# Kernel optimization log

Hardware: AMD Instinct MI355X
Metric: run time of the kernel (lower is better)

## Reference

```python
import jax, jax.numpy as jnp
import numpy as np

N = 100000
E = 3200000
NFEAT = 256
NHID = 128
NCLASS = 16
TEXT_CNT = 50000


def setup_inputs() -> dict:
    key = jax.random.key(0)
    ks = jax.random.split(key, 12)
    x = jax.random.normal(ks[0], (N, NFEAT), dtype=jnp.float32)
    adj_rows = jax.random.randint(ks[1], (E,), 0, N, dtype=jnp.int32)
    adj_cols = jax.random.randint(ks[2], (E,), 0, N, dtype=jnp.int32)
    # positive normalized-adjacency-like weights (~1/avg_degree scale)
    adj_vals = jax.random.uniform(ks[3], (E,), dtype=jnp.float32) / 32.0
    W1 = jax.random.normal(ks[4], (NFEAT, NHID), dtype=jnp.float32) / np.sqrt(NFEAT)
    b1 = jax.random.normal(ks[5], (NHID,), dtype=jnp.float32) * 0.01
    W2 = jax.random.normal(ks[6], (NHID, NFEAT), dtype=jnp.float32) / np.sqrt(NHID)
    b2 = jax.random.normal(ks[7], (NFEAT,), dtype=jnp.float32) * 0.01
    cW1 = jax.random.normal(ks[8], (NFEAT, NCLASS), dtype=jnp.float32) / np.sqrt(NFEAT)
    cb1 = jax.random.normal(ks[9], (NCLASS,), dtype=jnp.float32) * 0.01
    cW2 = jax.random.normal(ks[10], (NFEAT, NCLASS), dtype=jnp.float32) / np.sqrt(NFEAT)
    cb2 = jax.random.normal(ks[11], (NCLASS,), dtype=jnp.float32) * 0.01
    return {"x": x, "adj_rows": adj_rows, "adj_cols": adj_cols, "adj_vals": adj_vals,
            "W1": W1, "b1": b1, "W2": W2, "b2": b2,
            "cW1": cW1, "cb1": cb1, "cW2": cw2 if (cw2 := None) else cW2, "cb2": cb2}


def spmm(rows, cols, vals, dense):
    # out[r] = sum_{e: rows[e]==r} vals[e] * dense[cols[e]]   (COO SpMM)
    gathered = vals[:, None] * dense[cols]  # [E, D]
    return jax.ops.segment_sum(gathered, rows, num_segments=N)


def reference(x, adj_rows, adj_cols, adj_vals, W1, b1, W2, b2, cW1, cb1, cW2, cb2):
    # gc1: adj @ (x @ W1) + b1, then ReLU (dropout is identity at inference)
    h = jax.nn.relu(spmm(adj_rows, adj_cols, adj_vals, x @ W1) + b1)  # [N, NHID]
    # gc2: adj @ (h @ W2) + b2
    out = spmm(adj_rows, adj_cols, adj_vals, h @ W2) + b2  # [N, NFEAT]
    text_cls = out[:TEXT_CNT] @ cW1 + cb1  # [TEXT_CNT, NCLASS]
    img_cls = out[TEXT_CNT:] @ cW2 + cb2   # [N-TEXT_CNT, NCLASS]
    return (out, text_cls, img_cls)
```

## Files before the change

### kernel.cpp

```cpp
#include <hip/hip_runtime.h>

#define N_NODES  100000
#define N_EDGES  3200000
#define NFEAT    256
#define NHID     128
#define NCLASS   16
#define TEXT_CNT 50000

#define RPB      256
#define NB       ((N_NODES + RPB - 1) / RPB)
#define CAP      16384
#define SC_EDGES 8192
#define SC_BLKS  ((N_EDGES + SC_EDGES - 1) / SC_EDGES)
#define FN_CAPL  9216

typedef unsigned int uint;
typedef __bf16 bf16x8 __attribute__((ext_vector_type(8)));
typedef __bf16 bf16x4 __attribute__((ext_vector_type(4)));
typedef float f32x4 __attribute__((ext_vector_type(4)));

__device__ inline uint bf16_rne(float f) {
  uint u = __float_as_uint(f);
  return (u + 0x7fffu + ((u >> 16) & 1u)) >> 16;
}
__device__ inline float bf_lo(uint u) { return __uint_as_float(u << 16); }
__device__ inline float bf_hi(uint u) { return __uint_as_float(u & 0xffff0000u); }


__global__ __launch_bounds__(256) void prep_kernel(const float* __restrict__ W1,
                                                   const float* __restrict__ W2,
                                                   const float* __restrict__ b2,
                                                   const float* __restrict__ cW1,
                                                   const float* __restrict__ cb1,
                                                   const float* __restrict__ cW2,
                                                   const float* __restrict__ cb2,
                                                   unsigned short* __restrict__ W1t,
                                                   unsigned short* __restrict__ W2t,
                                                   float* __restrict__ Wc1, float* __restrict__ bc1,
                                                   float* __restrict__ Wc2, float* __restrict__ bc2,
                                                   int* __restrict__ gcursor) {
  int idx = blockIdx.x * 256 + threadIdx.x;
  if (idx < 32768) {
    int n = idx >> 8, k = idx & 255;
    W1t[idx] = (unsigned short)bf16_rne(W1[(size_t)k * NHID + n]);
  } else if (idx < 65536) {
    int i2 = idx - 32768;
    int n = i2 >> 7, k = i2 & 127;
    W2t[i2] = (unsigned short)bf16_rne(W2[(size_t)k * NFEAT + n]);
  } else if (idx < 69632) {
    int e = idx - 65536;
    int set = e >> 11;
    int e2 = e & 2047;
    int i = e2 >> 4, c = e2 & 15;
    const float* cw = set ? cW2 : cW1;
    float acc = 0.f;
    for (int k = 0; k < NFEAT; ++k)
      acc += W2[(size_t)i * NFEAT + k] * cw[k * NCLASS + c];
    (set ? Wc2 : Wc1)[e2] = acc;
    if (e < 32) {
      int s2 = e >> 4, c2 = e & 15;
      const float* cwb = s2 ? cW2 : cW1;
      float b = (s2 ? cb2 : cb1)[c2];
      for (int k = 0; k < NFEAT; ++k) b += b2[k] * cwb[k * NCLASS + c2];
      (s2 ? bc2 : bc1)[c2] = b;
    }
  } else if (idx < 69632 + NB) {
    int b = idx - 69632;
    gcursor[b] = b * CAP;
  }
}


__global__ __launch_bounds__(512) void scatter_sort_kernel(const int* __restrict__ rows,
                                                           const int* __restrict__ cols,
                                                           const float* __restrict__ vals,
                                                           int* __restrict__ gcursor,
                                                           int2* __restrict__ packedA, int E) {
  __shared__ int2 eds[SC_EDGES];
  __shared__ int hist[512];
  __shared__ int bcnt[NB];
  __shared__ int lofs[NB];
  __shared__ int lcur[NB];
  __shared__ int gofs[NB];
  int t = threadIdx.x;
  int base = blockIdx.x * SC_EDGES;
  hist[t] = 0;
  __syncthreads();
#pragma unroll
  for (int i = 0; i < SC_EDGES / 512; ++i) {
    int e = base + i * 512 + t;
    if (e < E) atomicAdd(&hist[rows[e] >> 8], 1);
  }
  __syncthreads();
  int v = hist[t];
  if (t < NB) bcnt[t] = v;
  __syncthreads();
  for (int off = 1; off < 512; off <<= 1) {
    int u = (t >= off) ? hist[t - off] : 0;
    __syncthreads();
    hist[t] += u;
    __syncthreads();
  }
  if (t < NB) {
    int ex = hist[t] - v;
    lofs[t] = ex;
    lcur[t] = ex;
    gofs[t] = v ? atomicAdd(&gcursor[t], v) : 0;
  }
  __syncthreads();
#pragma unroll
  for (int i = 0; i < SC_EDGES / 512; ++i) {
    int e = base + i * 512 + t;
    if (e < E) {
      int r = rows[e];
      int b = r >> 8;
      int p = atomicAdd(&lcur[b], 1);
      eds[p] = make_int2(((r & 255) << 17) | cols[e], __float_as_int(vals[e]));
    }
  }
  __syncthreads();
  int wid = t >> 6, lane = t & 63;
  for (int b = wid; b < NB; b += 8) {
    int cnt = bcnt[b];
    int lo = lofs[b];
    int go = gofs[b];
    int lim = (b + 1) << 14;
    for (int j = lane; j < cnt; j += 64)
      if (go + j < lim) packedA[go + j] = eds[lo + j];
  }
}


__global__ __launch_bounds__(512) void csr_finalize_kernel(const int* __restrict__ gcursor,
                                                           const int2* __restrict__ packedA,
                                                           int2* __restrict__ packedB,
                                                           int* __restrict__ row_ptr) {
  __shared__ int2 eds[FN_CAPL];
  __shared__ int pre[512];
  __shared__ int rh[RPB];
  __shared__ int rofs[RPB];
  __shared__ int rcur[RPB];
  int b = blockIdx.x;
  int t = threadIdx.x;
  int cntt = (t < NB) ? (gcursor[t] - t * CAP) : 0;
  pre[t] = cntt;
  __syncthreads();
  for (int off = 1; off < 512; off <<= 1) {
    int u = (t >= off) ? pre[t - off] : 0;
    __syncthreads();
    pre[t] += u;
    __syncthreads();
  }
  int cnt = gcursor[b] - b * CAP;
  int gout = pre[b] - cnt;
  int s0 = b * CAP;
  int end = s0 + cnt;
  if (t < RPB) rh[t] = 0;
  __syncthreads();
  for (int i = s0 + t; i < end; i += 512)
    atomicAdd(&rh[packedA[i].x >> 17], 1);
  __syncthreads();
  int v = (t < RPB) ? rh[t] : 0;
  if (t < RPB) rofs[t] = v;
  __syncthreads();
  for (int off = 1; off < RPB; off <<= 1) {
    int u = (t >= off && t < RPB) ? rofs[t - off] : 0;
    __syncthreads();
    if (t < RPB) rofs[t] += u;
    __syncthreads();
  }
  if (t < RPB) {
    int ex = rofs[t] - v;
    rcur[t] = ex;
    int row = b * RPB + t;
    if (row < N_NODES) row_ptr[row] = gout + ex;
  }
  if (b == 0 && t == 0) row_ptr[N_NODES] = N_EDGES;
  __syncthreads();
  if (cnt <= FN_CAPL) {
    for (int i = s0 + t; i < end; i += 512) {
      int2 pk = packedA[i];
      int p = atomicAdd(&rcur[pk.x >> 17], 1);
      eds[p] = pk;
    }
    __syncthreads();
    for (int i = t; i < cnt; i += 512) {
      int2 pk = eds[i];
      packedB[gout + i] = make_int2((pk.x & 0x1FFFF) << 8, pk.y);
    }
  } else {
    for (int i = s0 + t; i < end; i += 512) {
      int2 pk = packedA[i];
      int p = atomicAdd(&rcur[pk.x >> 17], 1);
      packedB[gout + p] = make_int2((pk.x & 0x1FFFF) << 8, pk.y);
    }
  }
}


template <int A_FP32, int OUT_BF16, int K, int N>
__device__ __forceinline__ void gemm_body(int bx, int by, const void* __restrict__ Aptr,
                                          const __bf16* __restrict__ Bt,
                                          const float* __restrict__ bias,
                                          void* __restrict__ Cptr, int M,
                                          __bf16* __restrict__ As, __bf16* __restrict__ Bs) {
  int tid = threadIdx.x;
  int lane = tid & 63;
  int w = tid >> 6;
  int wr = w >> 1, wc = w & 1;
  int brow = bx * 128;
  int bcol = by * 128;
  int r16 = lane & 15, kb = lane >> 4;

  f32x4 acc[4][4];
#pragma unroll
  for (int m = 0; m < 4; ++m)
#pragma unroll
    for (int n = 0; n < 4; ++n) acc[m][n] = (f32x4){0.f, 0.f, 0.f, 0.f};

  for (int k0 = 0; k0 < K; k0 += 32) {
    if (A_FP32) {
      const float* A = (const float*)Aptr;
#pragma unroll
      for (int i = 0; i < 4; ++i) {
        int idx = tid + i * 256;
        int row = idx >> 3;
        int kq = (idx & 7) << 2;
        int gr = brow + row;
        float4 v = make_float4(0.f, 0.f, 0.f, 0.f);
        if (gr < M) v = *(const float4*)&A[(size_t)gr * K + k0 + kq];
        bf16x4 o;
        o[0] = (__bf16)v.x; o[1] = (__bf16)v.y; o[2] = (__bf16)v.z; o[3] = (__bf16)v.w;
        *(bf16x4*)&As[row * 40 + kq] = o;
      }
    } else {
      const __bf16* A = (const __bf16*)Aptr;
#pragma unroll
      for (int i = 0; i < 2; ++i) {
        int idx = tid + i * 256;
        int row = idx >> 2;
        int kq = (idx & 3) << 3;
        int gr = brow + row;
        bf16x8 v = {};
        if (gr < M) v = *(const bf16x8*)&A[(size_t)gr * K + k0 + kq];
        *(bf16x8*)&As[row * 40 + kq] = v;
      }
    }
#pragma unroll
    for (int i = 0; i < 2; ++i) {
      int idx = tid + i * 256;
      int col = idx >> 2;
      int kq = (idx & 3) << 3;
      bf16x8 v = *(const bf16x8*)&Bt[(size_t)(bcol + col) * K + k0 + kq];
      *(bf16x8*)&Bs[col * 40 + kq] = v;
    }
    __syncthreads();

    bf16x8 a[4], b[4];
#pragma unroll
    for (int m = 0; m < 4; ++m)
      a[m] = *(bf16x8*)&As[(wr * 64 + m * 16 + r16) * 40 + kb * 8];
#pragma unroll
    for (int n = 0; n < 4; ++n)
      b[n] = *(bf16x8*)&Bs[(wc * 64 + n * 16 + r16) * 40 + kb * 8];
#pragma unroll
    for (int m = 0; m < 4; ++m)
#pragma unroll
      for (int n = 0; n < 4; ++n)
        acc[m][n] = __builtin_amdgcn_mfma_f32_16x16x32_bf16(a[m], b[n], acc[m][n], 0, 0, 0);
    __syncthreads();
  }

  int crow0 = brow + wr * 64;
  int ccol0 = bcol + wc * 64;
#pragma unroll
  for (int n = 0; n < 4; ++n) {
    int col = ccol0 + n * 16 + r16;
    float bv = bias ? bias[col] : 0.f;
#pragma unroll
    for (int m = 0; m < 4; ++m) {
#pragma unroll
      for (int r = 0; r < 4; ++r) {
        int row = crow0 + m * 16 + kb * 4 + r;
        if (row < M) {
          float val = acc[m][n][r] + bv;
          if (OUT_BF16)
            ((unsigned short*)Cptr)[(size_t)row * N + col] = (unsigned short)bf16_rne(val);
          else
            ((float*)Cptr)[(size_t)row * N + col] = val;
        }
      }
    }
  }
}


template <int A_FP32, int OUT_BF16, int K, int N>
__global__ __launch_bounds__(256) void gemm_mfma_kernel(const void* __restrict__ Aptr,
                                                        const __bf16* __restrict__ Bt,
                                                        const float* __restrict__ bias,
                                                        void* __restrict__ Cptr, int M) {
  __shared__ __align__(16) __bf16 smem[2 * 128 * 40];
  gemm_body<A_FP32, OUT_BF16, K, N>(blockIdx.x, blockIdx.y, Aptr, Bt, bias, Cptr, M,
                                    smem, smem + 128 * 40);
}


__global__ __launch_bounds__(256) void spmm_bf16_kernel(const int* __restrict__ row_ptr,
                                                        const int2* __restrict__ packed,
                                                        const uint* __restrict__ src,
                                                        uint* __restrict__ dst,
                                                        const float* __restrict__ bias,
                                                        int relu, int nrows) {
  int tid = threadIdx.x;
  int lane = tid & 63;
  int half = lane >> 5;
  int l32 = lane & 31;
  int row = blockIdx.x * 4 + (tid >> 6);
  if (row >= nrows) return;
  int s = row_ptr[row];
  int e = row_ptr[row + 1];
  const char* srcb = (const char*)src + (l32 << 3);
  float a0 = 0.f, a1 = 0.f, a2 = 0.f, a3 = 0.f;
  int i = s;
  for (; i + 16 <= e; i += 16) {
    int2 m0 = packed[i + 0 + half], m1 = packed[i + 2 + half];
    int2 m2 = packed[i + 4 + half], m3 = packed[i + 6 + half];
    int2 m4 = packed[i + 8 + half], m5 = packed[i + 10 + half];
    int2 m6 = packed[i + 12 + half], m7 = packed[i + 14 + half];
    uint2 u0 = *(const uint2*)(srcb + (uint)m0.x);
    uint2 u1 = *(const uint2*)(srcb + (uint)m1.x);
    uint2 u2 = *(const uint2*)(srcb + (uint)m2.x);
    uint2 u3 = *(const uint2*)(srcb + (uint)m3.x);
    uint2 u4 = *(const uint2*)(srcb + (uint)m4.x);
    uint2 u5 = *(const uint2*)(srcb + (uint)m5.x);
    uint2 u6 = *(const uint2*)(srcb + (uint)m6.x);
    uint2 u7 = *(const uint2*)(srcb + (uint)m7.x);
    float v0 = __int_as_float(m0.y), v1 = __int_as_float(m1.y);
    float v2 = __int_as_float(m2.y), v3 = __int_as_float(m3.y);
    float v4 = __int_as_float(m4.y), v5 = __int_as_float(m5.y);
    float v6 = __int_as_float(m6.y), v7 = __int_as_float(m7.y);
    a0 += v0 * bf_lo(u0.x); a1 += v0 * bf_hi(u0.x); a2 += v0 * bf_lo(u0.y); a3 += v0 * bf_hi(u0.y);
    a0 += v1 * bf_lo(u1.x); a1 += v1 * bf_hi(u1.x); a2 += v1 * bf_lo(u1.y); a3 += v1 * bf_hi(u1.y);
    a0 += v2 * bf_lo(u2.x); a1 += v2 * bf_hi(u2.x); a2 += v2 * bf_lo(u2.y); a3 += v2 * bf_hi(u2.y);
    a0 += v3 * bf_lo(u3.x); a1 += v3 * bf_hi(u3.x); a2 += v3 * bf_lo(u3.y); a3 += v3 * bf_hi(u3.y);
    a0 += v4 * bf_lo(u4.x); a1 += v4 * bf_hi(u4.x); a2 += v4 * bf_lo(u4.y); a3 += v4 * bf_hi(u4.y);
    a0 += v5 * bf_lo(u5.x); a1 += v5 * bf_hi(u5.x); a2 += v5 * bf_lo(u5.y); a3 += v5 * bf_hi(u5.y);
    a0 += v6 * bf_lo(u6.x); a1 += v6 * bf_hi(u6.x); a2 += v6 * bf_lo(u6.y); a3 += v6 * bf_hi(u6.y);
    a0 += v7 * bf_lo(u7.x); a1 += v7 * bf_hi(u7.x); a2 += v7 * bf_lo(u7.y); a3 += v7 * bf_hi(u7.y);
  }
  for (; i + 8 <= e; i += 8) {
    int2 m0 = packed[i + 0 + half], m1 = packed[i + 2 + half];
    int2 m2 = packed[i + 4 + half], m3 = packed[i + 6 + half];
    uint2 u0 = *(const uint2*)(srcb + (uint)m0.x);
    uint2 u1 = *(const uint2*)(srcb + (uint)m1.x);
    uint2 u2 = *(const uint2*)(srcb + (uint)m2.x);
    uint2 u3 = *(const uint2*)(srcb + (uint)m3.x);
    float v0 = __int_as_float(m0.y), v1 = __int_as_float(m1.y);
    float v2 = __int_as_float(m2.y), v3 = __int_as_float(m3.y);
    a0 += v0 * bf_lo(u0.x); a1 += v0 * bf_hi(u0.x); a2 += v0 * bf_lo(u0.y); a3 += v0 * bf_hi(u0.y);
    a0 += v1 * bf_lo(u1.x); a1 += v1 * bf_hi(u1.x); a2 += v1 * bf_lo(u1.y); a3 += v1 * bf_hi(u1.y);
    a0 += v2 * bf_lo(u2.x); a1 += v2 * bf_hi(u2.x); a2 += v2 * bf_lo(u2.y); a3 += v2 * bf_hi(u2.y);
    a0 += v3 * bf_lo(u3.x); a1 += v3 * bf_hi(u3.x); a2 += v3 * bf_lo(u3.y); a3 += v3 * bf_hi(u3.y);
  }
  for (; i + 4 <= e; i += 4) {
    int2 m0 = packed[i + 0 + half], m1 = packed[i + 2 + half];
    uint2 u0 = *(const uint2*)(srcb + (uint)m0.x);
    uint2 u1 = *(const uint2*)(srcb + (uint)m1.x);
    float v0 = __int_as_float(m0.y), v1 = __int_as_float(m1.y);
    a0 += v0 * bf_lo(u0.x); a1 += v0 * bf_hi(u0.x); a2 += v0 * bf_lo(u0.y); a3 += v0 * bf_hi(u0.y);
    a0 += v1 * bf_lo(u1.x); a1 += v1 * bf_hi(u1.x); a2 += v1 * bf_lo(u1.y); a3 += v1 * bf_hi(u1.y);
  }
  for (; i < e; i += 2) {
    int ee = i + half;
    int ok = ee < e;
    int2 m = packed[ok ? ee : (e - 1)];
    uint2 u = *(const uint2*)(srcb + (uint)m.x);
    float v = ok ? __int_as_float(m.y) : 0.f;
    a0 += v * bf_lo(u.x); a1 += v * bf_hi(u.x); a2 += v * bf_lo(u.y); a3 += v * bf_hi(u.y);
  }
  a0 += __shfl_xor(a0, 32); a1 += __shfl_xor(a1, 32);
  a2 += __shfl_xor(a2, 32); a3 += __shfl_xor(a3, 32);
  if (half == 0) {
    if (bias) {
      a0 += bias[4 * l32 + 0]; a1 += bias[4 * l32 + 1];
      a2 += bias[4 * l32 + 2]; a3 += bias[4 * l32 + 3];
    }
    if (relu) {
      a0 = fmaxf(a0, 0.f); a1 = fmaxf(a1, 0.f);
      a2 = fmaxf(a2, 0.f); a3 = fmaxf(a3, 0.f);
    }
    uint2 o;
    o.x = bf16_rne(a0) | (bf16_rne(a1) << 16);
    o.y = bf16_rne(a2) | (bf16_rne(a3) << 16);
    *(uint2*)&dst[(size_t)row * 64 + l32 * 2] = o;
  }
}


__device__ __forceinline__ void cls_body(int bid, int clsblks,
                                         const uint* __restrict__ t3,
                                         const float* __restrict__ Wc1,
                                         const float* __restrict__ bc1,
                                         const float* __restrict__ Wc2,
                                         const float* __restrict__ bc2,
                                         float* __restrict__ out1,
                                         float* __restrict__ out2) {
  int half = clsblks >> 1;
  int region = bid >= half;
  int b = region ? bid - half : bid;
  const float* Wc = region ? Wc2 : Wc1;
  const float* bc = region ? bc2 : bc1;
  float* outp = region ? out2 : out1;
  int row0 = region ? TEXT_CNT : 0;
  int nrows = region ? (N_NODES - TEXT_CNT) : TEXT_CNT;

  int lane = threadIdx.x & 63;
  int wav = b * 4 + (threadIdx.x >> 6);
  int nw = half * 4;
  int c = lane & 15;
  int kg = lane >> 4;
  float w[32];
#pragma unroll
  for (int j = 0; j < 32; ++j) w[j] = Wc[(kg * 32 + j) * NCLASS + c];
  float bcv = bc[c];
  for (int r = wav; r < nrows; r += nw) {
    const uint4* rp = (const uint4*)&t3[(size_t)(row0 + r) * 64 + kg * 16];
    float acc = 0.f;
#pragma unroll
    for (int q = 0; q < 4; ++q) {
      uint4 u = rp[q];
      acc += bf_lo(u.x) * w[q * 8 + 0] + bf_hi(u.x) * w[q * 8 + 1]
           + bf_lo(u.y) * w[q * 8 + 2] + bf_hi(u.y) * w[q * 8 + 3]
           + bf_lo(u.z) * w[q * 8 + 4] + bf_hi(u.z) * w[q * 8 + 5]
           + bf_lo(u.w) * w[q * 8 + 6] + bf_hi(u.w) * w[q * 8 + 7];
    }
    acc += __shfl_xor(acc, 16);
    acc += __shfl_xor(acc, 32);
    if (lane < 16) outp[(size_t)r * NCLASS + lane] = acc + bcv;
  }
}


__global__ __launch_bounds__(256) void fused_g2c_kernel(const uint* __restrict__ t3u,
                                                        const __bf16* __restrict__ W2t,
                                                        const float* __restrict__ b2,
                                                        float* __restrict__ outp,
                                                        const float* __restrict__ Wc1,
                                                        const float* __restrict__ bc1,
                                                        const float* __restrict__ Wc2,
                                                        const float* __restrict__ bc2,
                                                        float* __restrict__ out1,
                                                        float* __restrict__ out2,
                                                        int g2blks, int clsblks) {
  __shared__ __align__(16) __bf16 smem[2 * 128 * 40];
  if ((int)blockIdx.x < g2blks) {
    int bx = blockIdx.x >> 1;
    int by = blockIdx.x & 1;
    gemm_body<0, 0, NHID, NFEAT>(bx, by, t3u, W2t, b2, outp, N_NODES,
                                 smem, smem + 128 * 40);
  } else {
    cls_body(blockIdx.x - g2blks, clsblks, t3u, Wc1, bc1, Wc2, bc2, out1, out2);
  }
}


extern "C" void kernel_launch(void* const* d_in, const int* in_sizes, int n_in,
                              void* d_out, int out_size, void* d_ws, size_t ws_size,
                              hipStream_t stream) {
  const float* x     = (const float*)d_in[0];
  const int*   arows = (const int*)d_in[1];
  const int*   acols = (const int*)d_in[2];
  const float* avals = (const float*)d_in[3];
  const float* W1    = (const float*)d_in[4];
  const float* b1    = (const float*)d_in[5];
  const float* W2    = (const float*)d_in[6];
  const float* b2    = (const float*)d_in[7];
  const float* cW1   = (const float*)d_in[8];
  const float* cb1   = (const float*)d_in[9];
  const float* cW2   = (const float*)d_in[10];
  const float* cb2   = (const float*)d_in[11];
  float* outp = (float*)d_out;

  char* ws = (char*)d_ws;
  size_t off = 0;
  auto alloc = [&](size_t bytes) -> void* {
    void* p = ws + off;
    off += (bytes + 255) & ~(size_t)255;
    return p;
  };
  uint*  t1u     = (uint*) alloc((size_t)N_NODES * 64 * 4);
  uint*  hu      = (uint*) alloc((size_t)N_NODES * 64 * 4);
  uint*  t3u     = (uint*) alloc((size_t)N_NODES * 64 * 4);
  int2*  packedA = (int2*) alloc((size_t)NB * CAP * 8);
  int2*  packedB = (int2*) alloc((size_t)N_EDGES * 8);
  int*   gcursor = (int*)  alloc((size_t)NB * 4);
  int*   rowp    = (int*)  alloc((size_t)(N_NODES + 1) * 4);
  unsigned short* W1t = (unsigned short*)alloc((size_t)NHID * NFEAT * 2);
  unsigned short* W2t = (unsigned short*)alloc((size_t)NFEAT * NHID * 2);
  float* Wc1     = (float*)alloc(NHID * NCLASS * 4);
  float* Wc2     = (float*)alloc(NHID * NCLASS * 4);
  float* bc1     = (float*)alloc(64);
  float* bc2     = (float*)alloc(64);

  prep_kernel<<<(69632 + NB + 255) / 256, 256, 0, stream>>>(
      W1, W2, b2, cW1, cb1, cW2, cb2, W1t, W2t, Wc1, bc1, Wc2, bc2, gcursor);

  scatter_sort_kernel<<<SC_BLKS, 512, 0, stream>>>(arows, acols, avals, gcursor, packedA, N_EDGES);

  csr_finalize_kernel<<<NB, 512, 0, stream>>>(gcursor, packedA, packedB, rowp);

  int mblk = (N_NODES + 127) / 128;
  gemm_mfma_kernel<1, 1, NFEAT, NHID><<<dim3(mblk, 1), 256, 0, stream>>>(
      x, (const __bf16*)W1t, nullptr, t1u, N_NODES);
  spmm_bf16_kernel<<<(N_NODES + 3) / 4, 256, 0, stream>>>(rowp, packedB, t1u, hu, b1, 1, N_NODES);
  spmm_bf16_kernel<<<(N_NODES + 3) / 4, 256, 0, stream>>>(rowp, packedB, hu, t3u, nullptr, 0, N_NODES);
  int g2blks = mblk * 2;
  int clsblks = 2048;
  fused_g2c_kernel<<<g2blks + clsblks, 256, 0, stream>>>(
      t3u, (const __bf16*)W2t, b2, outp, Wc1, bc1, Wc2, bc2,
      outp + (size_t)N_NODES * NFEAT,
      outp + (size_t)N_NODES * NFEAT + (size_t)TEXT_CNT * NCLASS,
      g2blks, clsblks);
}
```

Measured before the change: 428.2 us.

## Software-pipeline SpMM gathers and sort edges within rows by column half

The SpMM inner loop becomes a software pipeline: edge metadata for the next batch is loaded while the gathers for the current batch are in flight, which hides the latency of the dependent index-then-gather chain. The CSR finalize step also sub-sorts each row's edges by whether the column falls in the lower or upper half of the node range, aiming for better cache locality in the gathers. The pipeline holds more live registers, and the finalize prefix scan widens from 256 to 512 entries.

```diff
diff --git a/kernel.cpp b/kernel.cpp
--- a/kernel.cpp
+++ b/kernel.cpp
@@ -13,6 +13,7 @@
 #define SC_EDGES 8192
 #define SC_BLKS  ((N_EDGES + SC_EDGES - 1) / SC_EDGES)
 #define FN_CAPL  9216
+#define COLHALF  (N_NODES / 2)
 
 typedef unsigned int uint;
 typedef __bf16 bf16x8 __attribute__((ext_vector_type(8)));
@@ -137,9 +138,9 @@
                                                            int* __restrict__ row_ptr) {
   __shared__ int2 eds[FN_CAPL];
   __shared__ int pre[512];
-  __shared__ int rh[RPB];
-  __shared__ int rofs[RPB];
-  __shared__ int rcur[RPB];
+  __shared__ int kh[512];
+  __shared__ int kofs[512];
+  __shared__ int kcur[512];
   int b = blockIdx.x;
   int t = threadIdx.x;
   int cntt = (t < NB) ? (gcursor[t] - t * CAP) : 0;
@@ -155,32 +156,36 @@
   int gout = pre[b] - cnt;
   int s0 = b * CAP;
   int end = s0 + cnt;
-  if (t < RPB) rh[t] = 0;
-  __syncthreads();
-  for (int i = s0 + t; i < end; i += 512)
-    atomicAdd(&rh[packedA[i].x >> 17], 1);
-  __syncthreads();
-  int v = (t < RPB) ? rh[t] : 0;
-  if (t < RPB) rofs[t] = v;
-  __syncthreads();
-  for (int off = 1; off < RPB; off <<= 1) {
-    int u = (t >= off && t < RPB) ? rofs[t - off] : 0;
-    __syncthreads();
-    if (t < RPB) rofs[t] += u;
-    __syncthreads();
-  }
+  kh[t] = 0;
+  __syncthreads();
+  for (int i = s0 + t; i < end; i += 512) {
+    int2 pk = packedA[i];
+    int key = ((pk.x >> 17) << 1) | ((pk.x & 0x1FFFF) >= COLHALF);
+    atomicAdd(&kh[key], 1);
+  }
+  __syncthreads();
+  int v = kh[t];
+  kofs[t] = v;
+  __syncthreads();
+  for (int off = 1; off < 512; off <<= 1) {
+    int u = (t >= off) ? kofs[t - off] : 0;
+    __syncthreads();
+    kofs[t] += u;
+    __syncthreads();
+  }
+  kcur[t] = kofs[t] - v;
+  __syncthreads();
   if (t < RPB) {
-    int ex = rofs[t] - v;
-    rcur[t] = ex;
     int row = b * RPB + t;
-    if (row < N_NODES) row_ptr[row] = gout + ex;
+    if (row < N_NODES) row_ptr[row] = gout + kcur[2 * t];
   }
   if (b == 0 && t == 0) row_ptr[N_NODES] = N_EDGES;
   __syncthreads();
   if (cnt <= FN_CAPL) {
     for (int i = s0 + t; i < end; i += 512) {
       int2 pk = packedA[i];
-      int p = atomicAdd(&rcur[pk.x >> 17], 1);
+      int key = ((pk.x >> 17) << 1) | ((pk.x & 0x1FFFF) >= COLHALF);
+      int p = atomicAdd(&kcur[key], 1);
       eds[p] = pk;
     }
     __syncthreads();
@@ -191,7 +196,8 @@
   } else {
     for (int i = s0 + t; i < end; i += 512) {
       int2 pk = packedA[i];
-      int p = atomicAdd(&rcur[pk.x >> 17], 1);
+      int key = ((pk.x >> 17) << 1) | ((pk.x & 0x1FFFF) >= COLHALF);
+      int p = atomicAdd(&kcur[key], 1);
       packedB[gout + p] = make_int2((pk.x & 0x1FFFF) << 8, pk.y);
     }
   }
@@ -305,6 +311,16 @@
                                     smem, smem + 128 * 40);
 }
 
+
+#define FMA4(Gv0, Gv1, Gv2, Gv3, Vv0, Vv1, Vv2, Vv3)                                   \
+  a0 += Vv0 * bf_lo(Gv0.x); a1 += Vv0 * bf_hi(Gv0.x);                                  \
+  a2 += Vv0 * bf_lo(Gv0.y); a3 += Vv0 * bf_hi(Gv0.y);                                  \
+  a0 += Vv1 * bf_lo(Gv1.x); a1 += Vv1 * bf_hi(Gv1.x);                                  \
+  a2 += Vv1 * bf_lo(Gv1.y); a3 += Vv1 * bf_hi(Gv1.y);                                  \
+  a0 += Vv2 * bf_lo(Gv2.x); a1 += Vv2 * bf_hi(Gv2.x);                                  \
+  a2 += Vv2 * bf_lo(Gv2.y); a3 += Vv2 * bf_hi(Gv2.y);                                  \
+  a0 += Vv3 * bf_lo(Gv3.x); a1 += Vv3 * bf_hi(Gv3.x);                                  \
+  a2 += Vv3 * bf_lo(Gv3.y); a3 += Vv3 * bf_hi(Gv3.y);
 
 __global__ __launch_bounds__(256) void spmm_bf16_kernel(const int* __restrict__ row_ptr,
                                                         const int2* __restrict__ packed,
@@ -323,31 +339,42 @@
   const char* srcb = (const char*)src + (l32 << 3);
   float a0 = 0.f, a1 = 0.f, a2 = 0.f, a3 = 0.f;
   int i = s;
-  for (; i + 16 <= e; i += 16) {
-    int2 m0 = packed[i + 0 + half], m1 = packed[i + 2 + half];
-    int2 m2 = packed[i + 4 + half], m3 = packed[i + 6 + half];
-    int2 m4 = packed[i + 8 + half], m5 = packed[i + 10 + half];
-    int2 m6 = packed[i + 12 + half], m7 = packed[i + 14 + half];
-    uint2 u0 = *(const uint2*)(srcb + (uint)m0.x);
-    uint2 u1 = *(const uint2*)(srcb + (uint)m1.x);
-    uint2 u2 = *(const uint2*)(srcb + (uint)m2.x);
-    uint2 u3 = *(const uint2*)(srcb + (uint)m3.x);
-    uint2 u4 = *(const uint2*)(srcb + (uint)m4.x);
-    uint2 u5 = *(const uint2*)(srcb + (uint)m5.x);
-    uint2 u6 = *(const uint2*)(srcb + (uint)m6.x);
-    uint2 u7 = *(const uint2*)(srcb + (uint)m7.x);
-    float v0 = __int_as_float(m0.y), v1 = __int_as_float(m1.y);
-    float v2 = __int_as_float(m2.y), v3 = __int_as_float(m3.y);
-    float v4 = __int_as_float(m4.y), v5 = __int_as_float(m5.y);
-    float v6 = __int_as_float(m6.y), v7 = __int_as_float(m7.y);
-    a0 += v0 * bf_lo(u0.x); a1 += v0 * bf_hi(u0.x); a2 += v0 * bf_lo(u0.y); a3 += v0 * bf_hi(u0.y);
-    a0 += v1 * bf_lo(u1.x); a1 += v1 * bf_hi(u1.x); a2 += v1 * bf_lo(u1.y); a3 += v1 * bf_hi(u1.y);
-    a0 += v2 * bf_lo(u2.x); a1 += v2 * bf_hi(u2.x); a2 += v2 * bf_lo(u2.y); a3 += v2 * bf_hi(u2.y);
-    a0 += v3 * bf_lo(u3.x); a1 += v3 * bf_hi(u3.x); a2 += v3 * bf_lo(u3.y); a3 += v3 * bf_hi(u3.y);
-    a0 += v4 * bf_lo(u4.x); a1 += v4 * bf_hi(u4.x); a2 += v4 * bf_lo(u4.y); a3 += v4 * bf_hi(u4.y);
-    a0 += v5 * bf_lo(u5.x); a1 += v5 * bf_hi(u5.x); a2 += v5 * bf_lo(u5.y); a3 += v5 * bf_hi(u5.y);
-    a0 += v6 * bf_lo(u6.x); a1 += v6 * bf_hi(u6.x); a2 += v6 * bf_lo(u6.y); a3 += v6 * bf_hi(u6.y);
-    a0 += v7 * bf_lo(u7.x); a1 += v7 * bf_hi(u7.x); a2 += v7 * bf_lo(u7.y); a3 += v7 * bf_hi(u7.y);
+
+  if (e - s >= 16) {
+    int2 A0 = packed[i + 0 + half], A1 = packed[i + 2 + half];
+    int2 A2 = packed[i + 4 + half], A3 = packed[i + 6 + half];
+    uint2 G0 = *(const uint2*)(srcb + (uint)A0.x);
+    uint2 G1 = *(const uint2*)(srcb + (uint)A1.x);
+    uint2 G2 = *(const uint2*)(srcb + (uint)A2.x);
+    uint2 G3 = *(const uint2*)(srcb + (uint)A3.x);
+    float W0 = __int_as_float(A0.y), W1 = __int_as_float(A1.y);
+    float W2 = __int_as_float(A2.y), W3 = __int_as_float(A3.y);
+    int2 B0 = packed[i + 8 + half], B1 = packed[i + 10 + half];
+    int2 B2 = packed[i + 12 + half], B3 = packed[i + 14 + half];
+    i += 16;
+    for (; i + 8 <= e; i += 8) {
+      uint2 H0 = *(const uint2*)(srcb + (uint)B0.x);
+      uint2 H1 = *(const uint2*)(srcb + (uint)B1.x);
+      uint2 H2 = *(const uint2*)(srcb + (uint)B2.x);
+      uint2 H3 = *(const uint2*)(srcb + (uint)B3.x);
+      float X0 = __int_as_float(B0.y), X1 = __int_as_float(B1.y);
+      float X2 = __int_as_float(B2.y), X3 = __int_as_float(B3.y);
+      B0 = packed[i + 0 + half]; B1 = packed[i + 2 + half];
+      B2 = packed[i + 4 + half]; B3 = packed[i + 6 + half];
+      FMA4(G0, G1, G2, G3, W0, W1, W2, W3)
+      G0 = H0; G1 = H1; G2 = H2; G3 = H3;
+      W0 = X0; W1 = X1; W2 = X2; W3 = X3;
+    }
+    FMA4(G0, G1, G2, G3, W0, W1, W2, W3)
+    {
+      uint2 H0 = *(const uint2*)(srcb + (uint)B0.x);
+      uint2 H1 = *(const uint2*)(srcb + (uint)B1.x);
+      uint2 H2 = *(const uint2*)(srcb + (uint)B2.x);
+      uint2 H3 = *(const uint2*)(srcb + (uint)B3.x);
+      float X0 = __int_as_float(B0.y), X1 = __int_as_float(B1.y);
+      float X2 = __int_as_float(B2.y), X3 = __int_as_float(B3.y);
+      FMA4(H0, H1, H2, H3, X0, X1, X2, X3)
+    }
   }
   for (; i + 8 <= e; i += 8) {
     int2 m0 = packed[i + 0 + half], m1 = packed[i + 2 + half];
@@ -358,10 +385,7 @@
     uint2 u3 = *(const uint2*)(srcb + (uint)m3.x);
     float v0 = __int_as_float(m0.y), v1 = __int_as_float(m1.y);
     float v2 = __int_as_float(m2.y), v3 = __int_as_float(m3.y);
-    a0 += v0 * bf_lo(u0.x); a1 += v0 * bf_hi(u0.x); a2 += v0 * bf_lo(u0.y); a3 += v0 * bf_hi(u0.y);
-    a0 += v1 * bf_lo(u1.x); a1 += v1 * bf_hi(u1.x); a2 += v1 * bf_lo(u1.y); a3 += v1 * bf_hi(u1.y);
-    a0 += v2 * bf_lo(u2.x); a1 += v2 * bf_hi(u2.x); a2 += v2 * bf_lo(u2.y); a3 += v2 * bf_hi(u2.y);
-    a0 += v3 * bf_lo(u3.x); a1 += v3 * bf_hi(u3.x); a2 += v3 * bf_lo(u3.y); a3 += v3 * bf_hi(u3.y);
+    FMA4(u0, u1, u2, u3, v0, v1, v2, v3)
   }
   for (; i + 4 <= e; i += 4) {
     int2 m0 = packed[i + 0 + half], m1 = packed[i + 2 + half];
```

Measured after the change: 427.8 us. No clear change (-0.1%).

## Split SpMM into feature-half passes and sort edges by column half within rows

Applied to the files above, without the earlier changes.

Each SpMM is split into two launches, each handling 64 of the 128 hidden features, so a gathered source row segment is 128 bytes and the working set of gathered data per pass is halved. Each wave now processes four edges per step across 16-lane groups, with an extra shuffle reduction. The CSR build also sorts edges within each row by whether the column falls in the lower or upper node half, so gathers within a row are grouped by address range. The cost is twice as many launches, twice as many reads of edge metadata, and a larger sort key histogram.

```diff
diff --git a/kernel.cpp b/kernel.cpp
--- a/kernel.cpp
+++ b/kernel.cpp
@@ -13,6 +13,7 @@
 #define SC_EDGES 8192
 #define SC_BLKS  ((N_EDGES + SC_EDGES - 1) / SC_EDGES)
 #define FN_CAPL  9216
+#define COLHALF  (N_NODES / 2)
 
 typedef unsigned int uint;
 typedef __bf16 bf16x8 __attribute__((ext_vector_type(8)));
@@ -137,9 +138,9 @@
                                                            int* __restrict__ row_ptr) {
   __shared__ int2 eds[FN_CAPL];
   __shared__ int pre[512];
-  __shared__ int rh[RPB];
-  __shared__ int rofs[RPB];
-  __shared__ int rcur[RPB];
+  __shared__ int kh[512];
+  __shared__ int kofs[512];
+  __shared__ int kcur[512];
   int b = blockIdx.x;
   int t = threadIdx.x;
   int cntt = (t < NB) ? (gcursor[t] - t * CAP) : 0;
@@ -155,32 +156,36 @@
   int gout = pre[b] - cnt;
   int s0 = b * CAP;
   int end = s0 + cnt;
-  if (t < RPB) rh[t] = 0;
-  __syncthreads();
-  for (int i = s0 + t; i < end; i += 512)
-    atomicAdd(&rh[packedA[i].x >> 17], 1);
-  __syncthreads();
-  int v = (t < RPB) ? rh[t] : 0;
-  if (t < RPB) rofs[t] = v;
-  __syncthreads();
-  for (int off = 1; off < RPB; off <<= 1) {
-    int u = (t >= off && t < RPB) ? rofs[t - off] : 0;
-    __syncthreads();
-    if (t < RPB) rofs[t] += u;
-    __syncthreads();
-  }
+  kh[t] = 0;
+  __syncthreads();
+  for (int i = s0 + t; i < end; i += 512) {
+    int2 pk = packedA[i];
+    int key = ((pk.x >> 17) << 1) | ((pk.x & 0x1FFFF) >= COLHALF);
+    atomicAdd(&kh[key], 1);
+  }
+  __syncthreads();
+  int v = kh[t];
+  kofs[t] = v;
+  __syncthreads();
+  for (int off = 1; off < 512; off <<= 1) {
+    int u = (t >= off) ? kofs[t - off] : 0;
+    __syncthreads();
+    kofs[t] += u;
+    __syncthreads();
+  }
+  kcur[t] = kofs[t] - v;
+  __syncthreads();
   if (t < RPB) {
-    int ex = rofs[t] - v;
-    rcur[t] = ex;
     int row = b * RPB + t;
-    if (row < N_NODES) row_ptr[row] = gout + ex;
+    if (row < N_NODES) row_ptr[row] = gout + kcur[2 * t];
   }
   if (b == 0 && t == 0) row_ptr[N_NODES] = N_EDGES;
   __syncthreads();
   if (cnt <= FN_CAPL) {
     for (int i = s0 + t; i < end; i += 512) {
       int2 pk = packedA[i];
-      int p = atomicAdd(&rcur[pk.x >> 17], 1);
+      int key = ((pk.x >> 17) << 1) | ((pk.x & 0x1FFFF) >= COLHALF);
+      int p = atomicAdd(&kcur[key], 1);
       eds[p] = pk;
     }
     __syncthreads();
@@ -191,7 +196,8 @@
   } else {
     for (int i = s0 + t; i < end; i += 512) {
       int2 pk = packedA[i];
-      int p = atomicAdd(&rcur[pk.x >> 17], 1);
+      int key = ((pk.x >> 17) << 1) | ((pk.x & 0x1FFFF) >= COLHALF);
+      int p = atomicAdd(&kcur[key], 1);
       packedB[gout + p] = make_int2((pk.x & 0x1FFFF) << 8, pk.y);
     }
   }
@@ -306,28 +312,32 @@
 }
 
 
-__global__ __launch_bounds__(256) void spmm_bf16_kernel(const int* __restrict__ row_ptr,
+#define FMAG(U, V)                                                   \
+  a0 += (V) * bf_lo((U).x); a1 += (V) * bf_hi((U).x);                \
+  a2 += (V) * bf_lo((U).y); a3 += (V) * bf_hi((U).y);
+
+__global__ __launch_bounds__(256) void spmm_half_kernel(const int* __restrict__ row_ptr,
                                                         const int2* __restrict__ packed,
                                                         const uint* __restrict__ src,
                                                         uint* __restrict__ dst,
                                                         const float* __restrict__ bias,
-                                                        int relu, int nrows) {
+                                                        int relu, int nrows, int h) {
   int tid = threadIdx.x;
   int lane = tid & 63;
-  int half = lane >> 5;
-  int l32 = lane & 31;
+  int q = lane >> 4;
+  int l16 = lane & 15;
   int row = blockIdx.x * 4 + (tid >> 6);
   if (row >= nrows) return;
   int s = row_ptr[row];
   int e = row_ptr[row + 1];
-  const char* srcb = (const char*)src + (l32 << 3);
+  const char* srcb = (const char*)src + (h << 7) + (l16 << 3);
   float a0 = 0.f, a1 = 0.f, a2 = 0.f, a3 = 0.f;
   int i = s;
-  for (; i + 16 <= e; i += 16) {
-    int2 m0 = packed[i + 0 + half], m1 = packed[i + 2 + half];
-    int2 m2 = packed[i + 4 + half], m3 = packed[i + 6 + half];
-    int2 m4 = packed[i + 8 + half], m5 = packed[i + 10 + half];
-    int2 m6 = packed[i + 12 + half], m7 = packed[i + 14 + half];
+  for (; i + 32 <= e; i += 32) {
+    int2 m0 = packed[i + 0 + q],  m1 = packed[i + 4 + q];
+    int2 m2 = packed[i + 8 + q],  m3 = packed[i + 12 + q];
+    int2 m4 = packed[i + 16 + q], m5 = packed[i + 20 + q];
+    int2 m6 = packed[i + 24 + q], m7 = packed[i + 28 + q];
     uint2 u0 = *(const uint2*)(srcb + (uint)m0.x);
     uint2 u1 = *(const uint2*)(srcb + (uint)m1.x);
     uint2 u2 = *(const uint2*)(srcb + (uint)m2.x);
@@ -340,51 +350,44 @@
     float v2 = __int_as_float(m2.y), v3 = __int_as_float(m3.y);
     float v4 = __int_as_float(m4.y), v5 = __int_as_float(m5.y);
     float v6 = __int_as_float(m6.y), v7 = __int_as_float(m7.y);
-    a0 += v0 * bf_lo(u0.x); a1 += v0 * bf_hi(u0.x); a2 += v0 * bf_lo(u0.y); a3 += v0 * bf_hi(u0.y);
-    a0 += v1 * bf_lo(u1.x); a1 += v1 * bf_hi(u1.x); a2 += v1 * bf_lo(u1.y); a3 += v1 * bf_hi(u1.y);
-    a0 += v2 * bf_lo(u2.x); a1 += v2 * bf_hi(u2.x); a2 += v2 * bf_lo(u2.y); a3 += v2 * bf_hi(u2.y);
-    a0 += v3 * bf_lo(u3.x); a1 += v3 * bf_hi(u3.x); a2 += v3 * bf_lo(u3.y); a3 += v3 * bf_hi(u3.y);
-    a0 += v4 * bf_lo(u4.x); a1 += v4 * bf_hi(u4.x); a2 += v4 * bf_lo(u4.y); a3 += v4 * bf_hi(u4.y);
-    a0 += v5 * bf_lo(u5.x); a1 += v5 * bf_hi(u5.x); a2 += v5 * bf_lo(u5.y); a3 += v5 * bf_hi(u5.y);
-    a0 += v6 * bf_lo(u6.x); a1 += v6 * bf_hi(u6.x); a2 += v6 * bf_lo(u6.y); a3 += v6 * bf_hi(u6.y);
-    a0 += v7 * bf_lo(u7.x); a1 += v7 * bf_hi(u7.x); a2 += v7 * bf_lo(u7.y); a3 += v7 * bf_hi(u7.y);
-  }
-  for (; i + 8 <= e; i += 8) {
-    int2 m0 = packed[i + 0 + half], m1 = packed[i + 2 + half];
-    int2 m2 = packed[i + 4 + half], m3 = packed[i + 6 + half];
+    FMAG(u0, v0) FMAG(u1, v1) FMAG(u2, v2) FMAG(u3, v3)
+    FMAG(u4, v4) FMAG(u5, v5) FMAG(u6, v6) FMAG(u7, v7)
+  }
+  for (; i + 16 <= e; i += 16) {
+    int2 m0 = packed[i + 0 + q], m1 = packed[i + 4 + q];
+    int2 m2 = packed[i + 8 + q], m3 = packed[i + 12 + q];
     uint2 u0 = *(const uint2*)(srcb + (uint)m0.x);
     uint2 u1 = *(const uint2*)(srcb + (uint)m1.x);
     uint2 u2 = *(const uint2*)(srcb + (uint)m2.x);
     uint2 u3 = *(const uint2*)(srcb + (uint)m3.x);
     float v0 = __int_as_float(m0.y), v1 = __int_as_float(m1.y);
     float v2 = __int_as_float(m2.y), v3 = __int_as_float(m3.y);
-    a0 += v0 * bf_lo(u0.x); a1 += v0 * bf_hi(u0.x); a2 += v0 * bf_lo(u0.y); a3 += v0 * bf_hi(u0.y);
-    a0 += v1 * bf_lo(u1.x); a1 += v1 * bf_hi(u1.x); a2 += v1 * bf_lo(u1.y); a3 += v1 * bf_hi(u1.y);
-    a0 += v2 * bf_lo(u2.x); a1 += v2 * bf_hi(u2.x); a2 += v2 * bf_lo(u2.y); a3 += v2 * bf_hi(u2.y);
-    a0 += v3 * bf_lo(u3.x); a1 += v3 * bf_hi(u3.x); a2 += v3 * bf_lo(u3.y); a3 += v3 * bf_hi(u3.y);
-  }
-  for (; i + 4 <= e; i += 4) {
-    int2 m0 = packed[i + 0 + half], m1 = packed[i + 2 + half];
+    FMAG(u0, v0) FMAG(u1, v1) FMAG(u2, v2) FMAG(u3, v3)
+  }
+  for (; i + 8 <= e; i += 8) {
+    int2 m0 = packed[i + 0 + q], m1 = packed[i + 4 + q];
     uint2 u0 = *(const uint2*)(srcb + (uint)m0.x);
     uint2 u1 = *(const uint2*)(srcb + (uint)m1.x);
     float v0 = __int_as_float(m0.y), v1 = __int_as_float(m1.y);
-    a0 += v0 * bf_lo(u0.x); a1 += v0 * bf_hi(u0.x); a2 += v0 * bf_lo(u0.y); a3 += v0 * bf_hi(u0.y);
-    a0 += v1 * bf_lo(u1.x); a1 += v1 * bf_hi(u1.x); a2 += v1 * bf_lo(u1.y); a3 += v1 * bf_hi(u1.y);
-  }
-  for (; i < e; i += 2) {
-    int ee = i + half;
+    FMAG(u0, v0) FMAG(u1, v1)
+  }
+  for (; i < e; i += 4) {
+    int ee = i + q;
     int ok = ee < e;
     int2 m = packed[ok ? ee : (e - 1)];
     uint2 u = *(const uint2*)(srcb + (uint)m.x);
     float v = ok ? __int_as_float(m.y) : 0.f;
-    a0 += v * bf_lo(u.x); a1 += v * bf_hi(u.x); a2 += v * bf_lo(u.y); a3 += v * bf_hi(u.y);
-  }
+    FMAG(u, v)
+  }
+  a0 += __shfl_xor(a0, 16); a1 += __shfl_xor(a1, 16);
+  a2 += __shfl_xor(a2, 16); a3 += __shfl_xor(a3, 16);
   a0 += __shfl_xor(a0, 32); a1 += __shfl_xor(a1, 32);
   a2 += __shfl_xor(a2, 32); a3 += __shfl_xor(a3, 32);
-  if (half == 0) {
+  if (q == 0) {
     if (bias) {
-      a0 += bias[4 * l32 + 0]; a1 += bias[4 * l32 + 1];
-      a2 += bias[4 * l32 + 2]; a3 += bias[4 * l32 + 3];
+      int f0 = (h << 6) + (l16 << 2);
+      a0 += bias[f0 + 0]; a1 += bias[f0 + 1];
+      a2 += bias[f0 + 2]; a3 += bias[f0 + 3];
     }
     if (relu) {
       a0 = fmaxf(a0, 0.f); a1 = fmaxf(a1, 0.f);
@@ -393,7 +396,7 @@
     uint2 o;
     o.x = bf16_rne(a0) | (bf16_rne(a1) << 16);
     o.y = bf16_rne(a2) | (bf16_rne(a3) << 16);
-    *(uint2*)&dst[(size_t)row * 64 + l32 * 2] = o;
+    *(uint2*)&dst[(size_t)row * 64 + (h << 5) + (l16 << 1)] = o;
   }
 }
 
@@ -428,12 +431,12 @@
     const uint4* rp = (const uint4*)&t3[(size_t)(row0 + r) * 64 + kg * 16];
     float acc = 0.f;
 #pragma unroll
-    for (int q = 0; q < 4; ++q) {
-      uint4 u = rp[q];
-      acc += bf_lo(u.x) * w[q * 8 + 0] + bf_hi(u.x) * w[q * 8 + 1]
-           + bf_lo(u.y) * w[q * 8 + 2] + bf_hi(u.y) * w[q * 8 + 3]
-           + bf_lo(u.z) * w[q * 8 + 4] + bf_hi(u.z) * w[q * 8 + 5]
-           + bf_lo(u.w) * w[q * 8 + 6] + bf_hi(u.w) * w[q * 8 + 7];
+    for (int qq = 0; qq < 4; ++qq) {
+      uint4 u = rp[qq];
+      acc += bf_lo(u.x) * w[qq * 8 + 0] + bf_hi(u.x) * w[qq * 8 + 1]
+           + bf_lo(u.y) * w[qq * 8 + 2] + bf_hi(u.y) * w[qq * 8 + 3]
+           + bf_lo(u.z) * w[qq * 8 + 4] + bf_hi(u.z) * w[qq * 8 + 5]
+           + bf_lo(u.w) * w[qq * 8 + 6] + bf_hi(u.w) * w[qq * 8 + 7];
     }
     acc += __shfl_xor(acc, 16);
     acc += __shfl_xor(acc, 32);
@@ -513,8 +516,13 @@
   int mblk = (N_NODES + 127) / 128;
   gemm_mfma_kernel<1, 1, NFEAT, NHID><<<dim3(mblk, 1), 256, 0, stream>>>(
       x, (const __bf16*)W1t, nullptr, t1u, N_NODES);
-  spmm_bf16_kernel<<<(N_NODES + 3) / 4, 256, 0, stream>>>(rowp, packedB, t1u, hu, b1, 1, N_NODES);
-  spmm_bf16_kernel<<<(N_NODES + 3) / 4, 256, 0, stream>>>(rowp, packedB, hu, t3u, nullptr, 0, N_NODES);
+
+  int sblk = (N_NODES + 3) / 4;
+  spmm_half_kernel<<<sblk, 256, 0, stream>>>(rowp, packedB, t1u, hu, b1, 1, N_NODES, 0);
+  spmm_half_kernel<<<sblk, 256, 0, stream>>>(rowp, packedB, t1u, hu, b1, 1, N_NODES, 1);
+  spmm_half_kernel<<<sblk, 256, 0, stream>>>(rowp, packedB, hu, t3u, nullptr, 0, N_NODES, 0);
+  spmm_half_kernel<<<sblk, 256, 0, stream>>>(rowp, packedB, hu, t3u, nullptr, 0, N_NODES, 1);
+
   int g2blks = mblk * 2;
   int clsblks = 2048;
   fused_g2c_kernel<<<g2blks + clsblks, 256, 0, stream>>>(
```

After: 449.9 us. 5.1% more time.
